# Kernel optimization log

Measured on AMD Instinct MI355X. Metric: run time of the kernel, lower is better.

## Reference

```python
import jax, jax.numpy as jnp
import numpy as np

T, D, H, J = 32768, 256, 64, 32


def setup_inputs() -> dict:
    key = jax.random.key(0)
    ks = jax.random.split(key, 6)
    states = jax.random.normal(ks[0], (T, D + 3), dtype=jnp.float32)
    h = jnp.zeros((H,), dtype=jnp.float32)
    # kaiming-normal (relu) init as in reset_parameters: std = sqrt(2/fan_in)
    w_ih = jax.random.normal(ks[1], (3 * H, D), dtype=jnp.float32) * np.float32((2.0 / D) ** 0.5)
    w_hh = jax.random.normal(ks[2], (3 * H, H), dtype=jnp.float32) * np.float32((2.0 / H) ** 0.5)
    b_ih = jnp.zeros((3 * H,), dtype=jnp.float32)
    b_hh = jnp.zeros((3 * H,), dtype=jnp.float32)
    w_out = jax.random.normal(ks[3], (J * J, H), dtype=jnp.float32) * np.float32((2.0 / H) ** 0.5)
    b_out = jnp.zeros((J * J,), dtype=jnp.float32)
    mask = jax.random.randint(ks[4], (J, J), 0, 2, dtype=jnp.int32)
    return {"states": states, "h": h, "w_ih": w_ih, "w_hh": w_hh,
            "b_ih": b_ih, "b_hh": b_hh, "w_out": w_out, "b_out": b_out, "mask": mask}


def reference(states, h, w_ih, w_hh, b_ih, b_hh, w_out, b_out, mask):
    # states: (T, D+3); last 3 columns dropped per original (states[t][:-3])
    x = states[:, :-3]                       # (T, D)
    # input-to-hidden projections have no recurrence -> precompute as one GEMM
    gi_all = x @ w_ih.T + b_ih               # (T, 3H)

    def step(h_prev, gi):
        gh = w_hh @ h_prev + b_hh            # (3H,)
        i_r, i_z, i_n = jnp.split(gi, 3)
        h_r, h_z, h_n = jnp.split(gh, 3)
        r = jax.nn.sigmoid(i_r + h_r)
        z = jax.nn.sigmoid(i_z + h_z)
        n = jnp.tanh(i_n + r * h_n)
        h_new = (1.0 - z) * n + z * h_prev   # torch GRUCell update
        return h_new, h_new

    h_final, hs = jax.lax.scan(step, h, gi_all)   # hs: (T, H)
    logits = (hs @ w_out.T + b_out).reshape(-1, J, J)   # (T, J, J)
    logits = jnp.where(mask == 0, jnp.float32(-1e9), logits)  # masked_fill
    return logits, h_final
```

## Files before the change

kernel.cpp:

```cpp
#include <hip/hip_runtime.h>

#define T_STEPS 32768
#define DIN 256
#define HID 64
#define G3 192
#define JJ 1024
#define PF 4

typedef float f4 __attribute__((ext_vector_type(4)));

__device__ __forceinline__ float hsum4(f4 v) { return (v.x + v.y) + (v.z + v.w); }

__device__ __forceinline__ float qsum(float v) {
    float a = __int_as_float(__builtin_amdgcn_mov_dpp(__float_as_int(v), 0xB1, 0xF, 0xF, true));
    float s = v + a;
    float b = __int_as_float(__builtin_amdgcn_mov_dpp(__float_as_int(s), 0x4E, 0xF, 0xF, true));
    return s + b;
}

__global__ __launch_bounds__(192)
void k_gi(const float* __restrict__ states, const float* __restrict__ w_ih,
          const float* __restrict__ b_ih, float* __restrict__ gi)
{
    __shared__ __align__(16) float xs[32 * DIN];
    const int tid  = threadIdx.x;
    const int row0 = blockIdx.x * 32;

    for (int i = tid; i < 32 * DIN; i += 192)
        xs[i] = states[(size_t)(row0 + (i >> 8)) * (DIN + 3) + (i & 255)];
    __syncthreads();

    const int c = tid;
    float acc[32];
#pragma unroll
    for (int r = 0; r < 32; ++r) acc[r] = 0.f;

    for (int k4 = 0; k4 < DIN / 4; ++k4) {
        const float4 wv = *(const float4*)&w_ih[c * DIN + k4 * 4];
#pragma unroll
        for (int r = 0; r < 32; ++r) {
            const float4 xv = *(const float4*)&xs[r * DIN + k4 * 4];
            acc[r] += xv.x * wv.x + xv.y * wv.y + xv.z * wv.z + xv.w * wv.w;
        }
    }
    const float bi = b_ih[c];
#pragma unroll
    for (int r = 0; r < 32; ++r)
        gi[(size_t)(row0 + r) * G3 + c] = acc[r] + bi;
}

__global__ __launch_bounds__(256)
void k_scan(const float* __restrict__ gi, const float* __restrict__ w_hh,
            const float* __restrict__ b_hh, const float* __restrict__ h0,
            float* __restrict__ hs, float* __restrict__ h_final)
{
    __shared__ __align__(16) float hsh[2][HID];

    const int tid = threadIdx.x;
    const int w   = tid >> 6;
    const int l   = tid & 63;
    const int e   = w * 16 + (l >> 2);
    const int c   = l & 3;
    const bool own = (c == 0);

    f4 wr0, wr1, wr2, wr3, wz0, wz1, wz2, wz3, wn0, wn1, wn2, wn3;
    {
        const float* r0 = w_hh + (size_t)e         * HID + c * 16;
        const float* r1 = w_hh + (size_t)(e + 64)  * HID + c * 16;
        const float* r2 = w_hh + (size_t)(e + 128) * HID + c * 16;
        wr0 = *(const f4*)&r0[0];  wr1 = *(const f4*)&r0[4];
        wr2 = *(const f4*)&r0[8];  wr3 = *(const f4*)&r0[12];
        wz0 = *(const f4*)&r1[0];  wz1 = *(const f4*)&r1[4];
        wz2 = *(const f4*)&r1[8];  wz3 = *(const f4*)&r1[12];
        wn0 = *(const f4*)&r2[0];  wn1 = *(const f4*)&r2[4];
        wn2 = *(const f4*)&r2[8];  wn3 = *(const f4*)&r2[12];
    }
    const float bhr = b_hh[e];
    const float bhz = b_hh[e + 64];
    const float bhn = b_hh[e + 128];

    const float LOG2E  =  1.44269504088896340736f;
    const float NLOG2E = -1.44269504088896340736f;
    const float L2E2   =  2.88539008177792681472f;
    const float crb  = NLOG2E * bhr;
    const float czb  = NLOG2E * bhz;
    const float bhn2 = L2E2 * bhn;

    float hv = h0[e];
    if (own) hsh[0][e] = hv;
    __syncthreads();

    float pr[PF], pz[PF], pn[PF];
#pragma unroll
    for (int j = 0; j < PF; ++j) {
        pr[j] = gi[(size_t)j * G3 + e];
        pz[j] = gi[(size_t)j * G3 + e + 64];
        pn[j] = gi[(size_t)j * G3 + e + 128];
    }

#pragma unroll PF
    for (int s = 0; s < T_STEPS; ++s) {
        const int j = s & (PF - 1);

        const float* hb = &hsh[s & 1][c * 16];
        const f4 hq0 = *(const f4*)&hb[0];
        const f4 hq1 = *(const f4*)&hb[4];
        const f4 hq2 = *(const f4*)&hb[8];
        const f4 hq3 = *(const f4*)&hb[12];

        const float gir = pr[j], giz = pz[j], gin = pn[j];

        const int sp = (s + PF) & (T_STEPS - 1);
        pr[j] = gi[(size_t)sp * G3 + e];
        pz[j] = gi[(size_t)sp * G3 + e + 64];
        pn[j] = gi[(size_t)sp * G3 + e + 128];

        f4 ar4 = wr0 * hq0;
        f4 az4 = wz0 * hq0;
        f4 an4 = wn0 * hq0;
        ar4 = __builtin_elementwise_fma(wr1, hq1, ar4);
        az4 = __builtin_elementwise_fma(wz1, hq1, az4);
        an4 = __builtin_elementwise_fma(wn1, hq1, an4);
        ar4 = __builtin_elementwise_fma(wr2, hq2, ar4);
        az4 = __builtin_elementwise_fma(wz2, hq2, az4);
        an4 = __builtin_elementwise_fma(wn2, hq2, an4);
        ar4 = __builtin_elementwise_fma(wr3, hq3, ar4);
        az4 = __builtin_elementwise_fma(wz3, hq3, az4);
        an4 = __builtin_elementwise_fma(wn3, hq3, an4);

        const float ar = qsum(hsum4(ar4));
        const float az = qsum(hsum4(az4));
        const float qn = qsum(hsum4(an4));

        const float cr   = __builtin_fmaf(NLOG2E, gir, crb);
        const float cz   = __builtin_fmaf(NLOG2E, giz, czb);
        const float gin2 = L2E2 * gin;
        const float an2  = __builtin_fmaf(qn, L2E2, bhn2);

        const float er = __builtin_amdgcn_exp2f(__builtin_fmaf(ar, NLOG2E, cr));
        const float r  = __builtin_amdgcn_rcpf(1.f + er);

        const float ez = __builtin_amdgcn_exp2f(__builtin_fmaf(az, NLOG2E, cz));
        const float z  = __builtin_amdgcn_rcpf(1.f + ez);
        const float zc  = 1.f - z;
        const float zhv = z * hv;

        const float u  = __builtin_amdgcn_exp2f(__builtin_fmaf(r, an2, gin2));
        const float wn = __builtin_amdgcn_rcpf(u + 1.f);
        const float n  = __builtin_fmaf(-2.f, wn, 1.f);

        hv = __builtin_fmaf(zc, n, zhv);

        if (own) {
            hsh[(s + 1) & 1][e] = hv;
            hs[(size_t)s * HID + e] = hv;
        }

        asm volatile("s_waitcnt lgkmcnt(0)\n\ts_barrier" ::: "memory");
    }
    if (own) h_final[e] = hv;
}

__global__ __launch_bounds__(256)
void k_out(const float* __restrict__ hs, const float* __restrict__ w_out,
           const float* __restrict__ b_out, const int* __restrict__ mask,
           float* __restrict__ out)
{
    __shared__ __align__(16) float hs_s[16 * HID];
    const int tid  = threadIdx.x;
    const int row0 = blockIdx.x * 16;

    {
        const float4 v = *(const float4*)&hs[(size_t)row0 * HID + tid * 4];
        *(float4*)&hs_s[tid * 4] = v;
    }
    __syncthreads();

    float acc[16][4];
#pragma unroll
    for (int r = 0; r < 16; ++r)
#pragma unroll
        for (int cc = 0; cc < 4; ++cc) acc[r][cc] = 0.f;

    for (int k4 = 0; k4 < HID / 4; ++k4) {
        float4 wv[4];
#pragma unroll
        for (int cc = 0; cc < 4; ++cc)
            wv[cc] = *(const float4*)&w_out[(size_t)(cc * 256 + tid) * HID + k4 * 4];
#pragma unroll
        for (int r = 0; r < 16; ++r) {
            const float4 hv = *(const float4*)&hs_s[r * HID + k4 * 4];
#pragma unroll
            for (int cc = 0; cc < 4; ++cc)
                acc[r][cc] += hv.x * wv[cc].x + hv.y * wv[cc].y +
                              hv.z * wv[cc].z + hv.w * wv[cc].w;
        }
    }

#pragma unroll
    for (int cc = 0; cc < 4; ++cc) {
        const int c = cc * 256 + tid;
        const float bo = b_out[c];
        const int m = mask[c];
#pragma unroll
        for (int r = 0; r < 16; ++r) {
            const float v = (m == 0) ? -1e9f : (acc[r][cc] + bo);
            out[(size_t)(row0 + r) * JJ + c] = v;
        }
    }
}

extern "C" void kernel_launch(void* const* d_in, const int* in_sizes, int n_in,
                              void* d_out, int out_size, void* d_ws, size_t ws_size,
                              hipStream_t stream)
{
    const float* states = (const float*)d_in[0];
    const float* h0     = (const float*)d_in[1];
    const float* w_ih   = (const float*)d_in[2];
    const float* w_hh   = (const float*)d_in[3];
    const float* b_ih   = (const float*)d_in[4];
    const float* b_hh   = (const float*)d_in[5];
    const float* w_out  = (const float*)d_in[6];
    const float* b_out  = (const float*)d_in[7];
    const int*   mask   = (const int*)d_in[8];

    float* out = (float*)d_out;
    float* gi  = (float*)d_ws;
    float* hs  = gi + (size_t)T_STEPS * G3;
    float* h_final = out + (size_t)T_STEPS * JJ;

    k_gi  <<<dim3(T_STEPS / 32), dim3(192), 0, stream>>>(states, w_ih, b_ih, gi);
    k_scan<<<dim3(1),            dim3(256), 0, stream>>>(gi, w_hh, b_hh, h0, hs, h_final);
    k_out <<<dim3(T_STEPS / 16), dim3(256), 0, stream>>>(hs, w_out, b_out, mask, out);
}
```

Before: 8.746 ms.

## Register-tile input projection GEMM with LDS-staged weight chunks

Rewrites the input-to-hidden GEMM kernel so each thread computes a 4x8 register tile instead of one column over 32 rows. Weight slices of 16 k-values are staged into padded shared memory, and the padded stride on the input tile avoids bank conflicts. The goal is to cut redundant global weight loads and raise arithmetic intensity. The cost is extra barriers per k-chunk. The total runtime is probably dominated by the sequential scan kernel, so the overall effect may be small.

```diff
diff --git a/kernel.cpp b/kernel.cpp
--- a/kernel.cpp
+++ b/kernel.cpp
@@ -18,35 +18,71 @@
     return s + b;
 }
 
+#define XS_STR 268
+#define WS_STR 20
+
 __global__ __launch_bounds__(192)
 void k_gi(const float* __restrict__ states, const float* __restrict__ w_ih,
           const float* __restrict__ b_ih, float* __restrict__ gi)
 {
-    __shared__ __align__(16) float xs[32 * DIN];
+    __shared__ __align__(16) float xs[32 * XS_STR];
+    __shared__ __align__(16) float ws[192 * WS_STR];
     const int tid  = threadIdx.x;
     const int row0 = blockIdx.x * 32;
 
     for (int i = tid; i < 32 * DIN; i += 192)
-        xs[i] = states[(size_t)(row0 + (i >> 8)) * (DIN + 3) + (i & 255)];
-    __syncthreads();
-
-    const int c = tid;
-    float acc[32];
-#pragma unroll
-    for (int r = 0; r < 32; ++r) acc[r] = 0.f;
-
-    for (int k4 = 0; k4 < DIN / 4; ++k4) {
-        const float4 wv = *(const float4*)&w_ih[c * DIN + k4 * 4];
-#pragma unroll
-        for (int r = 0; r < 32; ++r) {
-            const float4 xv = *(const float4*)&xs[r * DIN + k4 * 4];
-            acc[r] += xv.x * wv.x + xv.y * wv.y + xv.z * wv.z + xv.w * wv.w;
-        }
-    }
-    const float bi = b_ih[c];
-#pragma unroll
-    for (int r = 0; r < 32; ++r)
-        gi[(size_t)(row0 + r) * G3 + c] = acc[r] + bi;
+        xs[(i >> 8) * XS_STR + (i & 255)] =
+            states[(size_t)(row0 + (i >> 8)) * (DIN + 3) + (i & 255)];
+
+    const int cg = tid % 24;
+    const int rg = tid / 24;
+
+    float acc[4][8];
+#pragma unroll
+    for (int rr = 0; rr < 4; ++rr)
+#pragma unroll
+        for (int q = 0; q < 8; ++q) acc[rr][q] = 0.f;
+
+    for (int kc = 0; kc < DIN / 16; ++kc) {
+        __syncthreads();
+#pragma unroll
+        for (int i2 = 0; i2 < 4; ++i2) {
+            const int v  = tid + 192 * i2;
+            const int c  = v >> 2;
+            const int kq = v & 3;
+            *(float4*)&ws[c * WS_STR + kq * 4] =
+                *(const float4*)&w_ih[(size_t)c * DIN + kc * 16 + kq * 4];
+        }
+        __syncthreads();
+
+#pragma unroll
+        for (int k4 = 0; k4 < 4; ++k4) {
+            const int kb = kc * 16 + k4 * 4;
+            float4 xv[4];
+#pragma unroll
+            for (int rr = 0; rr < 4; ++rr)
+                xv[rr] = *(const float4*)&xs[(rg * 4 + rr) * XS_STR + kb];
+            float4 wv[8];
+#pragma unroll
+            for (int q = 0; q < 8; ++q)
+                wv[q] = *(const float4*)&ws[(cg + 24 * q) * WS_STR + k4 * 4];
+#pragma unroll
+            for (int rr = 0; rr < 4; ++rr)
+#pragma unroll
+                for (int q = 0; q < 8; ++q)
+                    acc[rr][q] += xv[rr].x * wv[q].x + xv[rr].y * wv[q].y +
+                                  xv[rr].z * wv[q].z + xv[rr].w * wv[q].w;
+        }
+    }
+
+#pragma unroll
+    for (int q = 0; q < 8; ++q) {
+        const int c = cg + 24 * q;
+        const float bi = b_ih[c];
+#pragma unroll
+        for (int rr = 0; rr < 4; ++rr)
+            gi[(size_t)(row0 + rg * 4 + rr) * G3 + c] = acc[rr][q] + bi;
+    }
 }
 
 __global__ __launch_bounds__(256)
```

Result: no change. 8.726 ms (-0.2%).
